# Kernel optimization log

Measured on AMD Instinct MI355X. Metric: run time of the kernel, lower is better.

Reference implementation:

```python
import jax, jax.numpy as jnp
import numpy as np

B, S, E, FFN, Q = 8, 2048, 512, 2048, 8


def setup_inputs() -> dict:
    key = jax.random.key(0)
    k0, k1, k2, k3 = jax.random.split(key, 4)
    x = jax.random.normal(k0, (B, S, E), dtype=jnp.float32)
    ry = jax.random.normal(k1, (Q,), dtype=jnp.float32)  # trainable RY angles
    w1 = jax.random.normal(k2, (FFN, Q), dtype=jnp.float32) / np.sqrt(Q).astype(np.float32)
    b1 = jnp.zeros((FFN,), dtype=jnp.float32)
    w2 = jax.random.normal(k3, (E, FFN), dtype=jnp.float32) / np.sqrt(FFN).astype(np.float32)
    b2 = jnp.zeros((E,), dtype=jnp.float32)
    return {"x": x, "ry": ry, "w1": w1, "b1": b1, "w2": w2, "b2": b2}


def reference(x, ry, w1, b1, w2, b2):
    # Quantum layer: each qubit i starts in |0>, gets RX(x[..., i]) then RY(ry[i]),
    # then PauliZ expectation. Product state => closed form <Z_i> = cos(x_i) * cos(ry_i).
    nq = ry.shape[0]
    z = jnp.cos(x[..., :nq]) * jnp.cos(ry)  # [B, S, Q]
    # dropout is identity in eval mode
    h = jnp.einsum("bsq,fq->bsf", z, w1) + b1  # fc1
    return jnp.einsum("bsf,ef->bse", jax.nn.relu(h), w2) + b2  # fc2
```

## Files before the change

### kernel.cpp

```cpp
#include <hip/hip_runtime.h>
#include <cstdint>
#include <cstddef>


typedef __attribute__((ext_vector_type(8))) short s16x8;
typedef __attribute__((ext_vector_type(4))) float f32x4;

__device__ __forceinline__ unsigned short f2bf(float f) {
  unsigned int u = __float_as_uint(f);
  unsigned int r = u + 0x7fffu + ((u >> 16) & 1u);
  return (unsigned short)(r >> 16);
}

__device__ __forceinline__ void async_copy16(const void* g, void* l) {
  __builtin_amdgcn_global_load_lds(
      (const __attribute__((address_space(1))) void*)(uintptr_t)g,
      (__attribute__((address_space(3))) void*)(unsigned int)(uintptr_t)l,
      16, 0, 0);
}

__global__ __launch_bounds__(256) void k_act(
    const float* __restrict__ x, const float* __restrict__ ry,
    const float* __restrict__ w1, const float* __restrict__ b1,
    unsigned short* __restrict__ act) {
  __shared__ float zsh[32][8];
  const int t = threadIdx.x;
  const int r0 = blockIdx.x * 32;

  {
    const int row = t >> 3, q = t & 7;
    zsh[row][q] = __cosf(x[(size_t)(r0 + row) * 512 + q]) * __cosf(ry[q]);
  }

  const int f0 = t * 8;
  float4 wv[16];
#pragma unroll
  for (int i = 0; i < 8; ++i) {
    const float* wr = w1 + (size_t)(f0 + i) * 8;
    wv[2 * i] = *(const float4*)wr;
    wv[2 * i + 1] = *(const float4*)(wr + 4);
  }
  float bb[8];
  {
    float4 b0 = *(const float4*)(b1 + f0);
    float4 b4 = *(const float4*)(b1 + f0 + 4);
    bb[0] = b0.x; bb[1] = b0.y; bb[2] = b0.z; bb[3] = b0.w;
    bb[4] = b4.x; bb[5] = b4.y; bb[6] = b4.z; bb[7] = b4.w;
  }
  __syncthreads();

#pragma unroll 4
  for (int row = 0; row < 32; ++row) {
    float z[8];
#pragma unroll
    for (int q = 0; q < 8; ++q) z[q] = zsh[row][q];
    unsigned short o[8];
#pragma unroll
    for (int i = 0; i < 8; ++i) {
      float4 a = wv[2 * i], b = wv[2 * i + 1];
      float h = bb[i];
      h += z[0] * a.x + z[1] * a.y + z[2] * a.z + z[3] * a.w;
      h += z[4] * b.x + z[5] * b.y + z[6] * b.z + z[7] * b.w;
      o[i] = f2bf(fmaxf(h, 0.0f));
    }
    uint4 pack;
    pack.x = o[0] | ((unsigned)o[1] << 16);
    pack.y = o[2] | ((unsigned)o[3] << 16);
    pack.z = o[4] | ((unsigned)o[5] << 16);
    pack.w = o[6] | ((unsigned)o[7] << 16);
    *(uint4*)(act + (size_t)(r0 + row) * 2048 + f0) = pack;
  }
}

__global__ __launch_bounds__(256) void k_w2(const float* __restrict__ w2,
                                            unsigned short* __restrict__ w2b) {
  size_t i = ((size_t)blockIdx.x * 256 + threadIdx.x) * 4;
  float4 v = *(const float4*)(w2 + i);
  uint2 p;
  p.x = f2bf(v.x) | ((unsigned)f2bf(v.y) << 16);
  p.y = f2bf(v.z) | ((unsigned)f2bf(v.w) << 16);
  *(uint2*)(w2b + i) = p;
}

__global__ __launch_bounds__(256) void k_gemm(
    const unsigned short* __restrict__ A, const unsigned short* __restrict__ Bw,
    const float* __restrict__ b2, float* __restrict__ C) {
  __shared__ unsigned short As[128 * 32];
  __shared__ unsigned short Bs[128 * 32];
  const int t = threadIdx.x;
  const int lane = t & 63;
  const int w = t >> 6;
  const int nblk_m = gridDim.x >> 2;
  const int mt = blockIdx.x % nblk_m;
  const int nt = blockIdx.x / nblk_m;
  const int r0 = mt * 128;
  const int c0 = nt * 128;

  const int cA1 = t, cA2 = t + 256;
  const unsigned short* gA1 = A + (size_t)(r0 + (cA1 >> 2)) * 2048 + (cA1 & 3) * 8;
  const unsigned short* gA2 = A + (size_t)(r0 + (cA2 >> 2)) * 2048 + (cA2 & 3) * 8;
  const unsigned short* gB1 = Bw + (size_t)(c0 + (cA1 >> 2)) * 2048 + (cA1 & 3) * 8;
  const unsigned short* gB2 = Bw + (size_t)(c0 + (cA2 >> 2)) * 2048 + (cA2 & 3) * 8;
  char* lA1 = (char*)As + cA1 * 16;
  char* lA2 = (char*)As + cA2 * 16;
  char* lB1 = (char*)Bs + cA1 * 16;
  char* lB2 = (char*)Bs + cA2 * 16;

  const int wm = (w >> 1) * 64;
  const int wn = (w & 1) * 64;
  const int fr = lane & 15;
  const int quad = lane >> 4;

  f32x4 acc[4][4];
#pragma unroll
  for (int i = 0; i < 4; ++i)
#pragma unroll
    for (int j = 0; j < 4; ++j) acc[i][j] = (f32x4){0.f, 0.f, 0.f, 0.f};

  const unsigned short* pAf = As + (wm + fr) * 32 + quad * 8;
  const unsigned short* pBf = Bs + (wn + fr) * 32 + quad * 8;

  for (int kt = 0; kt < 64; ++kt) {
    async_copy16(gA1, lA1);
    async_copy16(gA2, lA2);
    async_copy16(gB1, lB1);
    async_copy16(gB2, lB2);
    gA1 += 32; gA2 += 32; gB1 += 32; gB2 += 32;
    __syncthreads();
    s16x8 af[4], bf[4];
#pragma unroll
    for (int i = 0; i < 4; ++i) af[i] = *(const s16x8*)(pAf + i * 16 * 32);
#pragma unroll
    for (int j = 0; j < 4; ++j) bf[j] = *(const s16x8*)(pBf + j * 16 * 32);
#pragma unroll
    for (int i = 0; i < 4; ++i)
#pragma unroll
      for (int j = 0; j < 4; ++j)
        acc[i][j] = __builtin_amdgcn_mfma_f32_16x16x32_bf16(af[i], bf[j],
                                                            acc[i][j], 0, 0, 0);
    __syncthreads();
  }

  float bias[4];
#pragma unroll
  for (int j = 0; j < 4; ++j) bias[j] = b2[c0 + wn + j * 16 + fr];
#pragma unroll
  for (int i = 0; i < 4; ++i) {
    const int rbase = r0 + wm + i * 16 + quad * 4;
#pragma unroll
    for (int rr = 0; rr < 4; ++rr) {
      float* crow = C + (size_t)(rbase + rr) * 512;
#pragma unroll
      for (int j = 0; j < 4; ++j)
        crow[c0 + wn + j * 16 + fr] = acc[i][j][rr] + bias[j];
    }
  }
}

__global__ __launch_bounds__(256) void k_naive(
    const float* __restrict__ x, const float* __restrict__ ry,
    const float* __restrict__ w1, const float* __restrict__ b1,
    const float* __restrict__ w2, const float* __restrict__ b2,
    float* __restrict__ out) {
  __shared__ float zsh[8];
  __shared__ float acts[2048];
  const int r = blockIdx.x;
  const int t = threadIdx.x;
  if (t < 8) zsh[t] = __cosf(x[(size_t)r * 512 + t]) * __cosf(ry[t]);
  __syncthreads();
  float z[8];
#pragma unroll
  for (int q = 0; q < 8; ++q) z[q] = zsh[q];
#pragma unroll
  for (int i = 0; i < 8; ++i) {
    const int f = t * 8 + i;
    const float* wr = w1 + (size_t)f * 8;
    float4 a = *(const float4*)wr;
    float4 b = *(const float4*)(wr + 4);
    float h = b1[f] + z[0] * a.x + z[1] * a.y + z[2] * a.z + z[3] * a.w +
              z[4] * b.x + z[5] * b.y + z[6] * b.z + z[7] * b.w;
    acts[f] = fmaxf(h, 0.0f);
  }
  __syncthreads();
  for (int ee = 0; ee < 2; ++ee) {
    const int e = t + ee * 256;
    const float* wr = w2 + (size_t)e * 2048;
    float acc = b2[e];
    for (int f = 0; f < 2048; f += 4) {
      float4 wv = *(const float4*)(wr + f);
      float4 av = *(const float4*)(acts + f);
      acc += av.x * wv.x + av.y * wv.y + av.z * wv.z + av.w * wv.w;
    }
    out[(size_t)r * 512 + e] = acc;
  }
}

extern "C" void kernel_launch(void* const* d_in, const int* in_sizes, int n_in,
                              void* d_out, int out_size, void* d_ws,
                              size_t ws_size, hipStream_t stream) {
  const float* x  = (const float*)d_in[0];
  const float* ry = (const float*)d_in[1];
  const float* w1 = (const float*)d_in[2];
  const float* b1 = (const float*)d_in[3];
  const float* w2 = (const float*)d_in[4];
  const float* b2 = (const float*)d_in[5];
  float* out = (float*)d_out;

  const size_t M = 16384;
  const size_t w2b_bytes = (size_t)512 * 2048 * 2;

  size_t chunk = 0;
  if (ws_size > w2b_bytes)
    chunk = ((ws_size - w2b_bytes) / ((size_t)2048 * 2)) & ~(size_t)127;
  if (chunk == 0) {
    k_naive<<<dim3(16384), dim3(256), 0, stream>>>(x, ry, w1, b1, w2, b2, out);
    return;
  }
  if (chunk > M) chunk = M;

  unsigned short* w2b = (unsigned short*)d_ws;
  unsigned short* act = (unsigned short*)((char*)d_ws + w2b_bytes);

  k_w2<<<dim3(1024), dim3(256), 0, stream>>>(w2, w2b);
  for (size_t r0 = 0; r0 < M; r0 += chunk) {
    const size_t rows = (M - r0 < chunk) ? (M - r0) : chunk;
    k_act<<<dim3((unsigned)(rows / 32)), dim3(256), 0, stream>>>(
        x + r0 * 512, ry, w1, b1, act);
    k_gemm<<<dim3((unsigned)(rows / 128) * 4), dim3(256), 0, stream>>>(
        act, w2b, b2, out + r0 * 512);
  }
}
```

Before: 154.9 us.

## Fuse fc1 activation computation into the fc2 MFMA GEMM main loop

Removes the separate activation kernel and its bf16 activation buffer. Each GEMM block now computes cos-features for its 128 rows and produces the ReLU(fc1) tile for every K step directly into LDS, with w1 slices double-buffered in shared memory. The output tile widens to 128x256 with 512 threads, giving 256 blocks. This avoids writing and re-reading the large intermediate activation matrix. In exchange, fc1 is recomputed by both column-half blocks, and with one 512-thread block per CU there is little latency hiding.

```diff
diff --git a/kernel.cpp b/kernel.cpp
--- a/kernel.cpp
+++ b/kernel.cpp
@@ -17,59 +17,6 @@
       (const __attribute__((address_space(1))) void*)(uintptr_t)g,
       (__attribute__((address_space(3))) void*)(unsigned int)(uintptr_t)l,
       16, 0, 0);
-}
-
-__global__ __launch_bounds__(256) void k_act(
-    const float* __restrict__ x, const float* __restrict__ ry,
-    const float* __restrict__ w1, const float* __restrict__ b1,
-    unsigned short* __restrict__ act) {
-  __shared__ float zsh[32][8];
-  const int t = threadIdx.x;
-  const int r0 = blockIdx.x * 32;
-
-  {
-    const int row = t >> 3, q = t & 7;
-    zsh[row][q] = __cosf(x[(size_t)(r0 + row) * 512 + q]) * __cosf(ry[q]);
-  }
-
-  const int f0 = t * 8;
-  float4 wv[16];
-#pragma unroll
-  for (int i = 0; i < 8; ++i) {
-    const float* wr = w1 + (size_t)(f0 + i) * 8;
-    wv[2 * i] = *(const float4*)wr;
-    wv[2 * i + 1] = *(const float4*)(wr + 4);
-  }
-  float bb[8];
-  {
-    float4 b0 = *(const float4*)(b1 + f0);
-    float4 b4 = *(const float4*)(b1 + f0 + 4);
-    bb[0] = b0.x; bb[1] = b0.y; bb[2] = b0.z; bb[3] = b0.w;
-    bb[4] = b4.x; bb[5] = b4.y; bb[6] = b4.z; bb[7] = b4.w;
-  }
-  __syncthreads();
-
-#pragma unroll 4
-  for (int row = 0; row < 32; ++row) {
-    float z[8];
-#pragma unroll
-    for (int q = 0; q < 8; ++q) z[q] = zsh[row][q];
-    unsigned short o[8];
-#pragma unroll
-    for (int i = 0; i < 8; ++i) {
-      float4 a = wv[2 * i], b = wv[2 * i + 1];
-      float h = bb[i];
-      h += z[0] * a.x + z[1] * a.y + z[2] * a.z + z[3] * a.w;
-      h += z[4] * b.x + z[5] * b.y + z[6] * b.z + z[7] * b.w;
-      o[i] = f2bf(fmaxf(h, 0.0f));
-    }
-    uint4 pack;
-    pack.x = o[0] | ((unsigned)o[1] << 16);
-    pack.y = o[2] | ((unsigned)o[3] << 16);
-    pack.z = o[4] | ((unsigned)o[5] << 16);
-    pack.w = o[6] | ((unsigned)o[7] << 16);
-    *(uint4*)(act + (size_t)(r0 + row) * 2048 + f0) = pack;
-  }
 }
 
 __global__ __launch_bounds__(256) void k_w2(const float* __restrict__ w2,
@@ -82,32 +29,65 @@
   *(uint2*)(w2b + i) = p;
 }
 
-__global__ __launch_bounds__(256) void k_gemm(
-    const unsigned short* __restrict__ A, const unsigned short* __restrict__ Bw,
-    const float* __restrict__ b2, float* __restrict__ C) {
+__global__ __launch_bounds__(512) void k_fused(
+    const float* __restrict__ x, const float* __restrict__ ry,
+    const float* __restrict__ w1, const float* __restrict__ b1,
+    const unsigned short* __restrict__ w2b, const float* __restrict__ b2,
+    float* __restrict__ C) {
   __shared__ unsigned short As[128 * 32];
-  __shared__ unsigned short Bs[128 * 32];
+  __shared__ unsigned short Bs[256 * 32];
+  __shared__ float w1s[2][8][32];
+  __shared__ float b1s[2048];
+
   const int t = threadIdx.x;
   const int lane = t & 63;
   const int w = t >> 6;
-  const int nblk_m = gridDim.x >> 2;
-  const int mt = blockIdx.x % nblk_m;
-  const int nt = blockIdx.x / nblk_m;
+  const int mt = (int)(blockIdx.x >> 1);
+  const int nt = (int)(blockIdx.x & 1);
   const int r0 = mt * 128;
-  const int c0 = nt * 128;
-
-  const int cA1 = t, cA2 = t + 256;
-  const unsigned short* gA1 = A + (size_t)(r0 + (cA1 >> 2)) * 2048 + (cA1 & 3) * 8;
-  const unsigned short* gA2 = A + (size_t)(r0 + (cA2 >> 2)) * 2048 + (cA2 & 3) * 8;
-  const unsigned short* gB1 = Bw + (size_t)(c0 + (cA1 >> 2)) * 2048 + (cA1 & 3) * 8;
-  const unsigned short* gB2 = Bw + (size_t)(c0 + (cA2 >> 2)) * 2048 + (cA2 & 3) * 8;
-  char* lA1 = (char*)As + cA1 * 16;
-  char* lA2 = (char*)As + cA2 * 16;
-  char* lB1 = (char*)Bs + cA1 * 16;
-  char* lB2 = (char*)Bs + cA2 * 16;
-
-  const int wm = (w >> 1) * 64;
-  const int wn = (w & 1) * 64;
+  const int c0 = nt * 256;
+
+  const int arow = t >> 2;
+  const int k8 = (t & 3) * 8;
+
+  float z[8];
+  {
+    const float* xr = x + (size_t)(r0 + arow) * 512;
+    float4 x0 = *(const float4*)xr;
+    float4 x1 = *(const float4*)(xr + 4);
+    float4 ra = *(const float4*)ry;
+    float4 rb = *(const float4*)(ry + 4);
+    z[0] = __cosf(x0.x) * __cosf(ra.x);
+    z[1] = __cosf(x0.y) * __cosf(ra.y);
+    z[2] = __cosf(x0.z) * __cosf(ra.z);
+    z[3] = __cosf(x0.w) * __cosf(ra.w);
+    z[4] = __cosf(x1.x) * __cosf(rb.x);
+    z[5] = __cosf(x1.y) * __cosf(rb.y);
+    z[6] = __cosf(x1.z) * __cosf(rb.z);
+    z[7] = __cosf(x1.w) * __cosf(rb.w);
+  }
+  {
+    float4 v = *(const float4*)(b1 + t * 4);
+    *(float4*)&b1s[t * 4] = v;
+  }
+  if (t < 64) {
+    float4 v = *(const float4*)(w1 + t * 4);
+    const int fl = t >> 1, q0 = (t & 1) * 4;
+    w1s[0][q0 + 0][fl] = v.x;
+    w1s[0][q0 + 1][fl] = v.y;
+    w1s[0][q0 + 2][fl] = v.z;
+    w1s[0][q0 + 3][fl] = v.w;
+  }
+  __syncthreads();
+
+  const unsigned short* gB1 =
+      w2b + (size_t)(c0 + (t >> 2)) * 2048 + (t & 3) * 8;
+  const unsigned short* gB2 = gB1 + (size_t)128 * 2048;
+  char* lB1 = (char*)Bs + t * 16;
+  char* lB2 = lB1 + 512 * 16;
+
+  const int wm = (w >> 2) * 64;
+  const int wn = (w & 3) * 64;
   const int fr = lane & 15;
   const int quad = lane >> 4;
 
@@ -119,24 +99,64 @@
 
   const unsigned short* pAf = As + (wm + fr) * 32 + quad * 8;
   const unsigned short* pBf = Bs + (wn + fr) * 32 + quad * 8;
+  unsigned short* pAw = As + arow * 32 + k8;
 
   for (int kt = 0; kt < 64; ++kt) {
-    async_copy16(gA1, lA1);
-    async_copy16(gA2, lA2);
+    const int cur = kt & 1;
+
     async_copy16(gB1, lB1);
     async_copy16(gB2, lB2);
-    gA1 += 32; gA2 += 32; gB1 += 32; gB2 += 32;
+    gB1 += 32;
+    gB2 += 32;
+    float4 wpre;
+    const bool do_w1 = (t < 64) && (kt < 63);
+    if (do_w1) wpre = *(const float4*)(w1 + (kt + 1) * 256 + t * 4);
+
+    float h[8];
+    {
+      float4 b0 = *(const float4*)&b1s[kt * 32 + k8];
+      float4 b4 = *(const float4*)&b1s[kt * 32 + k8 + 4];
+      h[0] = b0.x; h[1] = b0.y; h[2] = b0.z; h[3] = b0.w;
+      h[4] = b4.x; h[5] = b4.y; h[6] = b4.z; h[7] = b4.w;
+    }
+#pragma unroll
+    for (int q = 0; q < 8; ++q) {
+      float4 wa = *(const float4*)&w1s[cur][q][k8];
+      float4 wb = *(const float4*)&w1s[cur][q][k8 + 4];
+      h[0] += z[q] * wa.x; h[1] += z[q] * wa.y;
+      h[2] += z[q] * wa.z; h[3] += z[q] * wa.w;
+      h[4] += z[q] * wb.x; h[5] += z[q] * wb.y;
+      h[6] += z[q] * wb.z; h[7] += z[q] * wb.w;
+    }
+    unsigned short o[8];
+#pragma unroll
+    for (int j = 0; j < 8; ++j) o[j] = f2bf(fmaxf(h[j], 0.0f));
+    uint4 pk;
+    pk.x = o[0] | ((unsigned)o[1] << 16);
+    pk.y = o[2] | ((unsigned)o[3] << 16);
+    pk.z = o[4] | ((unsigned)o[5] << 16);
+    pk.w = o[6] | ((unsigned)o[7] << 16);
+    *(uint4*)pAw = pk;
+    if (do_w1) {
+      const int fl = t >> 1, q0 = (t & 1) * 4;
+      const int nxt = cur ^ 1;
+      w1s[nxt][q0 + 0][fl] = wpre.x;
+      w1s[nxt][q0 + 1][fl] = wpre.y;
+      w1s[nxt][q0 + 2][fl] = wpre.z;
+      w1s[nxt][q0 + 3][fl] = wpre.w;
+    }
     __syncthreads();
-    s16x8 af[4], bf[4];
+
+    s16x8 af[4], bfv[4];
 #pragma unroll
     for (int i = 0; i < 4; ++i) af[i] = *(const s16x8*)(pAf + i * 16 * 32);
 #pragma unroll
-    for (int j = 0; j < 4; ++j) bf[j] = *(const s16x8*)(pBf + j * 16 * 32);
+    for (int j = 0; j < 4; ++j) bfv[j] = *(const s16x8*)(pBf + j * 16 * 32);
 #pragma unroll
     for (int i = 0; i < 4; ++i)
 #pragma unroll
       for (int j = 0; j < 4; ++j)
-        acc[i][j] = __builtin_amdgcn_mfma_f32_16x16x32_bf16(af[i], bf[j],
+        acc[i][j] = __builtin_amdgcn_mfma_f32_16x16x32_bf16(af[i], bfv[j],
                                                             acc[i][j], 0, 0, 0);
     __syncthreads();
   }
@@ -206,27 +226,12 @@
   const float* b2 = (const float*)d_in[5];
   float* out = (float*)d_out;
 
-  const size_t M = 16384;
   const size_t w2b_bytes = (size_t)512 * 2048 * 2;
-
-  size_t chunk = 0;
-  if (ws_size > w2b_bytes)
-    chunk = ((ws_size - w2b_bytes) / ((size_t)2048 * 2)) & ~(size_t)127;
-  if (chunk == 0) {
+  if (ws_size < w2b_bytes) {
     k_naive<<<dim3(16384), dim3(256), 0, stream>>>(x, ry, w1, b1, w2, b2, out);
     return;
   }
-  if (chunk > M) chunk = M;
-
   unsigned short* w2b = (unsigned short*)d_ws;
-  unsigned short* act = (unsigned short*)((char*)d_ws + w2b_bytes);
-
   k_w2<<<dim3(1024), dim3(256), 0, stream>>>(w2, w2b);
-  for (size_t r0 = 0; r0 < M; r0 += chunk) {
-    const size_t rows = (M - r0 < chunk) ? (M - r0) : chunk;
-    k_act<<<dim3((unsigned)(rows / 32)), dim3(256), 0, stream>>>(
-        x + r0 * 512, ry, w1, b1, act);
-    k_gemm<<<dim3((unsigned)(rows / 128) * 4), dim3(256), 0, stream>>>(
-        act, w2b, b2, out + r0 * 512);
-  }
-}
+  k_fused<<<dim3(256), dim3(512), 0, stream>>>(x, ry, w1, b1, w2b, b2, out);
+}
```

After: 168.4 us. 8.7% more time.
